# Performance work log

Hardware: AMD Instinct MI355X
Metric: run time of the kernel (lower is better)

Reference implementation:

```python
import jax, jax.numpy as jnp
import numpy as np

N_HEAD = 16


def _rope_tables(T, head_dim, dtype):
    # RotaryEmbedding buffers: freqs = outer(t, inv_freq), half-dim tables [T, head_dim//2]
    inv_freq = 1.0 / (10000.0 ** (jnp.arange(0, head_dim, 2, dtype=jnp.float32) / head_dim))
    freqs = jnp.arange(T, dtype=jnp.float32)[:, None] * inv_freq[None, :]
    return jnp.cos(freqs).astype(dtype), jnp.sin(freqs).astype(dtype)


def _apply_rotary(x, cos, sin):
    # x: [B,H,T,D]; cos/sin: [T,D//2] broadcast over B,H
    d = x.shape[-1] // 2
    x1, x2 = x[..., :d], x[..., d:]
    return jnp.concatenate([x1 * cos - x2 * sin, x2 * cos + x1 * sin], axis=-1)


def setup_inputs() -> dict:
    key = jax.random.key(0)
    k1, k2, k3 = jax.random.split(key, 3)
    B, T, C = 2, 2048, 2048
    x = jax.random.normal(k1, (B, T, C), dtype=jnp.float32)
    Wqkv = jax.random.normal(k2, (C, 3 * C), dtype=jnp.float32) * (1.0 / np.sqrt(C))
    Wproj = jax.random.normal(k3, (C, C), dtype=jnp.float32) * (1.0 / np.sqrt(C))
    return {"x": x, "Wqkv": Wqkv, "Wproj": Wproj}


def reference(x, Wqkv, Wproj):
    B, T, C = x.shape
    H = N_HEAD
    D = C // H
    qkv = (x @ Wqkv).reshape(B, T, 3, H, D)
    q, k, v = qkv[:, :, 0], qkv[:, :, 1], qkv[:, :, 2]  # [B,T,H,D]
    q = jnp.transpose(q, (0, 2, 1, 3))  # [B,H,T,D]
    k = jnp.transpose(k, (0, 2, 1, 3))
    v = jnp.transpose(v, (0, 2, 1, 3))
    cos, sin = _rope_tables(T, D, x.dtype)
    q = _apply_rotary(q, cos, sin)
    k = _apply_rotary(k, cos, sin)
    scale = 1.0 / np.sqrt(D)
    scores = jnp.einsum('bhqd,bhkd->bhqk', q, k) * scale
    causal = jnp.tril(jnp.ones((T, T), dtype=bool))
    scores = jnp.where(causal, scores, jnp.finfo(scores.dtype).min)
    attn = jax.nn.softmax(scores, axis=-1)
    out = jnp.einsum('bhqk,bhkd->bhqd', attn, v)
    out = jnp.transpose(out, (0, 2, 1, 3)).reshape(B, T, C)
    return out @ Wproj
```

## Files before the change

kernel.cpp:

```cpp
#include <hip/hip_runtime.h>
#include <hip/hip_bf16.h>

typedef short s16b;
using bf16x4 = __attribute__((ext_vector_type(4))) short;
using bf16x8 = __attribute__((ext_vector_type(8))) short;
using f32x4  = __attribute__((ext_vector_type(4))) float;
using u32x4  = __attribute__((ext_vector_type(4))) unsigned;

#define DEVINL __device__ __forceinline__

DEVINL float bf2f(short u) {
    union { float f; unsigned u; } x;
    x.u = ((unsigned)(unsigned short)u) << 16;
    return x.f;
}
DEVINL short f2bf(float f) {
    unsigned u = __builtin_bit_cast(unsigned, f);
    u += 0x7FFFu + ((u >> 16) & 1u);
    return (short)(u >> 16);
}
DEVINL unsigned cvtpk(float a, float b) {
    unsigned r;
    asm("v_cvt_pk_bf16_f32 %0, %1, %2" : "=v"(r) : "v"(a), "v"(b));
    return r;
}

DEVINL f32x4 mfma16(bf16x8 a, bf16x8 b, f32x4 c) {
    return __builtin_amdgcn_mfma_f32_16x16x32_bf16(a, b, c, 0, 0, 0);
}

DEVINL void gload_lds16(const void* g, void* lds_uniform) {
    __builtin_amdgcn_global_load_lds(
        (const __attribute__((address_space(1))) char*)(const char*)g,
        (__attribute__((address_space(3))) char*)(char*)lds_uniform, 16, 0, 0);
}

DEVINL int perm32(int k) {
    return ((k >> 2) & 3) * 8 + ((k >> 4) & 1) * 4 + (k & 3);
}

DEVINL bf16x8 lds128(const s16b* base, int row, int ks, int g) {
    const char* p = (const char*)base + row * 128 + ((((ks << 2) + g) ^ (row & 7)) << 4);
    return *(const bf16x8*)p;
}
DEVINL bf16x8 lds256(const s16b* base, int row, int ds, int g) {
    const char* p = (const char*)base + row * 256 + ((((ds << 2) + g) ^ (row & 7)) << 4);
    return *(const bf16x8*)p;
}

__global__ void k_tables(float* __restrict__ ctab, float* __restrict__ stab) {
    int idx = blockIdx.x * 256 + threadIdx.x;
    int i = idx & 63, t = idx >> 6;
    float inv = powf(10000.0f, -(float)i * (1.0f / 64.0f));
    float fr = (float)t * inv;
    ctab[idx] = cosf(fr);
    stab[idx] = sinf(fr);
}

__global__ void k_cvt_x(const float* __restrict__ x, s16b* __restrict__ xb) {
    int idx = blockIdx.x * 256 + threadIdx.x;
    int p = idx * 4;
    int row = p >> 11, pc = p & 2047;
    int grp = pc >> 5, sp = pc & 31;
    int c = sp >> 3, half = (sp >> 2) & 1;
    int ksrc = grp * 32 + half * 16 + c * 4;
    float4 v = *(const float4*)(x + (size_t)row * 2048 + ksrc);
    bf16x4 o;
    o[0] = f2bf(v.x); o[1] = f2bf(v.y); o[2] = f2bf(v.z); o[3] = f2bf(v.w);
    *(bf16x4*)(xb + (size_t)row * 2048 + pc) = o;
}

__global__ void k_tcvt(const float* __restrict__ in, s16b* __restrict__ out, int R, int C) {
    __shared__ float tile[32][33];
    int tx = threadIdx.x & 31, ty = threadIdx.x >> 5;
    int c0 = blockIdx.x * 32, r0 = blockIdx.y * 32;
#pragma unroll
    for (int kk = 0; kk < 4; ++kk) {
        int r = ty + kk * 8;
        tile[r][tx] = in[(size_t)(r0 + r) * C + c0 + tx];
    }
    __syncthreads();
#pragma unroll
    for (int kk = 0; kk < 4; ++kk) {
        int r = ty + kk * 8;
        out[(size_t)(c0 + r) * R + r0 + perm32(tx)] = f2bf(tile[tx][r]);
    }
}

#define STG_B01(DB, KB)                                                        \
  gload_lds16(srcB + (KB), lds + 49152 + (DB) * 32768 + tid16);                \
  gload_lds16(srcB + 262144 + (KB), lds + 49152 + (DB) * 32768 + 8192 + tid16);
#define STG_B23(DB, KB)                                                        \
  gload_lds16(srcB + 524288 + (KB), lds + 49152 + (DB) * 32768 + 16384 + tid16); \
  gload_lds16(srcB + 786432 + (KB), lds + 49152 + (DB) * 32768 + 24576 + tid16);
#define STG_A01(DB, KB)                                                        \
  gload_lds16(srcA + (KB), lds + (DB) * 16384 + tid16);                        \
  gload_lds16(srcA + 262144 + (KB), lds + (DB) * 16384 + 8192 + tid16);

#define AF_READ(B, KS)                                                         \
    _Pragma("unroll")                                                          \
    for (int fi = 0; fi < 4; ++fi) {                                           \
      int row = (fi >> 1) * 64 + wm * 32 + (fi & 1) * 16 + r15;                \
      af[fi] = *(const bf16x8*)(lds + (B) * 16384 + row * 128                  \
               + ((((KS) * 4 + g) ^ (row & 7)) << 4));                         \
    }

#define PH4(B, KH, JH, STGC, WN)                                               \
  {                                                                            \
    if ((JH) == 0) { AF_READ(B, KH) }                                          \
    _Pragma("unroll")                                                          \
    for (int fj = 0; fj < 2; ++fj) {                                           \
      int row = (JH) * 128 + wn * 32 + fj * 16 + r15;                          \
      bfr[fj] = *(const bf16x8*)(lds + 49152 + (B) * 32768 + row * 128         \
                + ((((KH) * 4 + g) ^ (row & 7)) << 4));                        \
    }                                                                          \
    STGC                                                                       \
    if ((WN) == 6) { asm volatile("s_waitcnt vmcnt(6)" ::: "memory");          \
                     __builtin_amdgcn_sched_barrier(0); }                      \
    else if ((WN) == 0) { asm volatile("s_waitcnt vmcnt(0)" ::: "memory");     \
                     __builtin_amdgcn_sched_barrier(0); }                      \
    __builtin_amdgcn_s_barrier();                                              \
    asm volatile("s_waitcnt lgkmcnt(0)" ::: "memory");                         \
    __builtin_amdgcn_sched_barrier(0);                                         \
    __builtin_amdgcn_s_setprio(1);                                             \
    _Pragma("unroll")                                                          \
    for (int fi = 0; fi < 4; ++fi)                                             \
      _Pragma("unroll")                                                        \
      for (int fj = 0; fj < 2; ++fj)                                           \
        acc[fi][(JH) * 2 + fj] = mfma16(af[fi], bfr[fj], acc[fi][(JH) * 2 + fj]); \
    __builtin_amdgcn_s_setprio(0);                                             \
    __builtin_amdgcn_s_barrier();                                              \
    __builtin_amdgcn_sched_barrier(0);                                         \
  }

#define DO_TILE3(B, S1, S2, S3, WNL)                                           \
    PH4(B, 0, 0, S1, -1)                                                       \
    PH4(B, 0, 1, S2, -1)                                                       \
    PH4(B, 1, 0, S3, -1)                                                       \
    PH4(B, 1, 1, , WNL)

#define GEMM3_MAINLOOP(A_, B_)                                                 \
    __shared__ __attribute__((aligned(16))) char lds[147456];                  \
    const int tid = threadIdx.x;                                               \
    const int lane = tid & 63, wave = tid >> 6;                                \
    const int g = lane >> 4, r15 = lane & 15;                                  \
    const int wm = wave >> 2, wn = wave & 3;                                   \
    const int tid16 = tid << 4;                                                \
    const int rowL = tid16 >> 7;                                               \
    const int swzL = ((((tid16 >> 4) & 7) ^ (rowL & 7)) << 4);                 \
    const char* srcA = (const char*)(A_) + (size_t)(bm + rowL) * 4096 + swzL;  \
    const char* srcB = (const char*)(B_) + (size_t)(bn + rowL) * 4096 + swzL;  \
    f32x4 acc[4][4] = {};                                                      \
    bf16x8 af[4], bfr[2];                                                      \
    STG_B01(0, 0) STG_A01(0, 0) STG_B23(0, 0)                                  \
    STG_B01(1, 128) STG_A01(1, 128) STG_B23(1, 128)                            \
    asm volatile("s_waitcnt vmcnt(6)" ::: "memory");                           \
    __builtin_amdgcn_sched_barrier(0);                                         \
    __builtin_amdgcn_s_barrier();                                              \
    for (int t3 = 0; t3 < 10; ++t3) {                                          \
        const int kb2 = (3 * t3 + 2) * 128;                                    \
        const int kb3 = kb2 + 128, kb4 = kb2 + 256;                            \
        DO_TILE3(0, STG_B01(2, kb2), STG_A01(2, kb2), STG_B23(2, kb2), 6)      \
        DO_TILE3(1, STG_B01(0, kb3), STG_A01(0, kb3), STG_B23(0, kb3), 6)      \
        DO_TILE3(2, STG_B01(1, kb4), STG_A01(1, kb4), STG_B23(1, kb4), 6)      \
    }                                                                          \
    DO_TILE3(0, , , , 0)                                                       \
    DO_TILE3(1, , , , -1)

__global__ __launch_bounds__(512) void k_gemm_qkv(
    const s16b* __restrict__ A, const s16b* __restrict__ Bt,
    s16b* __restrict__ Qb, s16b* __restrict__ Kp, s16b* __restrict__ Vt,
    const float* __restrict__ ctab, const float* __restrict__ stab) {
    const int bid = blockIdx.x;
    const int xcd = bid & 7, local = bid >> 3;
    const int rr_ = local >> 5, w = local & 31;
    const int bm = ((xcd & 3) * 8 + (w >> 2)) * 128;
    const int bn = ((xcd >> 2) * 12 + rr_ * 4 + (w & 3)) * 256;
    GEMM3_MAINLOOP(A, Bt)
    const int which = bn >> 11;
    if (which < 2) {
        char* sml = (char*)lds;
#pragma unroll
        for (int i = 0; i < 4; ++i) {
#pragma unroll
            for (int j = 0; j < 4; ++j) {
                int mb0 = (i >> 1) * 64 + wm * 32 + (i & 1) * 16 + 4 * g;
                int nn = (j >> 1) * 128 + wn * 32 + (j & 1) * 16 + r15;
#pragma unroll
                for (int e = 0; e < 4; ++e) {
                    int mm = mb0 + e;
                    *(s16b*)(sml + mm * 528 + ((nn * 2) ^ ((mm & 3) << 5))) =
                        f2bf(acc[i][j][e]);
                }
            }
        }
        __syncthreads();
        const int mrow = tid >> 2, c4 = tid & 3;
        const int bb = bm >> 11;
        const int tt = (bm & 2047) + mrow;
        const char* srow = sml + mrow * 528;
        const int sw = (mrow & 3) << 5;
        bf16x8 v[8];
#pragma unroll
        for (int k = 0; k < 8; ++k) {
            int lc = c4 + 4 * k;
            v[k] = *(const bf16x8*)(srow + ((lc * 16) ^ sw));
        }
        float cs[2][8], sn[2][8];
#pragma unroll
        for (int j = 0; j < 2; ++j) {
            int d0 = 8 * c4 + 32 * j;
            const float* cp = ctab + tt * 64 + d0;
            const float* sp = stab + tt * 64 + d0;
            *(float4*)&cs[j][0] = *(const float4*)cp;
            *(float4*)&cs[j][4] = *(const float4*)(cp + 4);
            *(float4*)&sn[j][0] = *(const float4*)sp;
            *(float4*)&sn[j][4] = *(const float4*)(sp + 4);
        }
        if (which == 0) {
            const float SC = 0.12751744154f;
#pragma unroll
            for (int j = 0; j < 2; ++j)
#pragma unroll
                for (int e = 0; e < 8; ++e) { cs[j][e] *= SC; sn[j][e] *= SC; }
        }
        bf16x8 o[8];
#pragma unroll
        for (int hh = 0; hh < 2; ++hh)
#pragma unroll
            for (int j = 0; j < 2; ++j) {
                int kl = hh * 4 + j, kh = kl + 2;
                bf16x8 r1, r2;
#pragma unroll
                for (int e = 0; e < 8; ++e) {
                    float c = cs[j][e], s = sn[j][e];
                    float x1 = bf2f(v[kl][e]), x2 = bf2f(v[kh][e]);
                    r1[e] = f2bf(x1 * c - x2 * s);
                    r2[e] = f2bf(x2 * c + x1 * s);
                }
                o[kl] = r1; o[kh] = r2;
            }
        if (which == 0) {
#pragma unroll
            for (int k = 0; k < 8; ++k) {
                int lc = c4 + 4 * k;
                int ng = bn + lc * 8;
                int h = (ng >> 7) & 15, d = ng & 127;
                *(bf16x8*)(Qb + ((size_t)(bb * 16 + h) * 2048 + tt) * 128 + d) = o[k];
            }
        } else {
#pragma unroll
            for (int k = 0; k < 8; ++k) {
                int lc = c4 + 4 * k;
                int ng = bn + lc * 8;
                int h = (ng >> 7) & 15, d = ng & 127;
                size_t base = ((size_t)(bb * 16 + h) * 2048 + tt) * 128 + (d & ~31);
                int w2 = d & 31;
                bf16x4 lo, hi;
#pragma unroll
                for (int e = 0; e < 4; ++e) { lo[e] = o[k][e]; hi[e] = o[k][e + 4]; }
                *(bf16x4*)(Kp + base + perm32(w2)) = lo;
                *(bf16x4*)(Kp + base + perm32(w2 + 4)) = hi;
            }
        }
    } else {
#pragma unroll
        for (int i = 0; i < 4; ++i) {
            int m0 = bm + (i >> 1) * 64 + wm * 32 + (i & 1) * 16 + 4 * g;
            int b = m0 >> 11, t0 = m0 & 2047;
            int pt = (t0 & ~31) + perm32(t0 & 31);
#pragma unroll
            for (int j = 0; j < 4; ++j) {
                int n = bn + (j >> 1) * 128 + wn * 32 + (j & 1) * 16 + r15;
                int h = (n >> 7) & 15, d = n & 127;
                size_t base = ((size_t)(b * 16 + h) * 128 + d) * 2048 + pt;
                bf16x4 pk;
#pragma unroll
                for (int e = 0; e < 4; ++e) pk[e] = f2bf(acc[i][j][e]);
                *(bf16x4*)(Vt + base) = pk;
            }
        }
    }
}

__global__ __launch_bounds__(512) void k_gemm_proj(
    const s16b* __restrict__ A, const s16b* __restrict__ Bt, float* __restrict__ Co) {
    const int bid = blockIdx.x;
    const int xcd = bid & 7, local = bid >> 3;
    const int bm = (xcd * 4 + (local & 3)) * 128;
    const int bn = (local >> 2) * 256;
    GEMM3_MAINLOOP(A, Bt)
#pragma unroll
    for (int i = 0; i < 4; ++i) {
        int m0 = bm + (i >> 1) * 64 + wm * 32 + (i & 1) * 16 + 4 * g;
#pragma unroll
        for (int j = 0; j < 4; ++j) {
            int n = bn + (j >> 1) * 128 + wn * 32 + (j & 1) * 16 + r15;
#pragma unroll
            for (int e = 0; e < 4; ++e) Co[(size_t)(m0 + e) * 2048 + n] = acc[i][j][e];
        }
    }
}

__global__ __launch_bounds__(256) void k_attn(
    const s16b* __restrict__ Qb, const s16b* __restrict__ Kp,
    const s16b* __restrict__ Vt, s16b* __restrict__ AO) {
    __shared__ alignas(16) s16b Ks[2][64 * 128];
    __shared__ alignas(16) s16b Vs[2][128 * 64];
    const int tid = threadIdx.x;
    const int lane = tid & 63, wave = tid >> 6;
    const int g = lane >> 4, r15 = lane & 15;
    const int bh = blockIdx.x, pp = blockIdx.y;
    const s16b* Qg = Qb + (size_t)bh * 2048 * 128;
    const char* Kg = (const char*)(Kp + (size_t)bh * 2048 * 128);
    const char* Vg = (const char*)(Vt + (size_t)bh * 128 * 2048);
    const int b = bh >> 4, h = bh & 15;

#define ASTG(BUF, KT)                                                          \
    {                                                                          \
      const int k0s = (KT) * 64;                                               \
      _Pragma("unroll")                                                        \
      for (int rr = 0; rr < 4; ++rr) {                                         \
        int uo = (rr * 256 + wave * 64) * 16;                                  \
        int o = uo + lane * 16;                                                \
        {                                                                      \
          int row = o >> 8, sl = (o >> 4) & 15;                                \
          int sg = (sl ^ (row & 7)) << 4;                                      \
          gload_lds16(Kg + (size_t)(k0s + row) * 256 + sg,                     \
                      (char*)Ks + (BUF) * 16384 + uo);                         \
        }                                                                      \
        {                                                                      \
          int row = o >> 7, sl = (o >> 4) & 7;                                 \
          int sg = (sl ^ (row & 7)) << 4;                                      \
          gload_lds16(Vg + (size_t)row * 4096 + (size_t)k0s * 2 + sg,          \
                      (char*)Vs + (BUF) * 16384 + uo);                         \
        }                                                                      \
      }                                                                        \
    }

    for (int pass = 0; pass < 2; ++pass) {
        const int qt = pass ? pp : (15 - pp);
        const int q0 = qt * 128 + wave * 32;
        const int ktiles = qt * 2 + 2;

        ASTG(0, 0)

        bf16x8 qf[2][4];
#pragma unroll
        for (int qs = 0; qs < 2; ++qs)
#pragma unroll
            for (int ds = 0; ds < 4; ++ds) {
                const s16b* p = Qg + (size_t)(q0 + qs * 16 + r15) * 128 + ds * 32 + 4 * g;
                bf16x4 lo = *(const bf16x4*)p;
                bf16x4 hi = *(const bf16x4*)(p + 16);
                qf[qs][ds] = __builtin_shufflevector(lo, hi, 0, 1, 2, 3, 4, 5, 6, 7);
            }

        f32x4 ot[8][2] = {};
        float m_s[2] = {-3e38f, -3e38f};
        float l_s[2] = {0.f, 0.f};

        for (int kt = 0; kt < ktiles; ++kt) {
            const int k0 = kt * 64;
            if (kt + 1 < ktiles) {
                ASTG((kt + 1) & 1, kt + 1)
                asm volatile("s_waitcnt vmcnt(8)" ::: "memory");
            } else {
                asm volatile("s_waitcnt vmcnt(0)" ::: "memory");
            }
            __builtin_amdgcn_sched_barrier(0);
            __builtin_amdgcn_s_barrier();
            asm volatile("" ::: "memory");
            __builtin_amdgcn_sched_barrier(0);

            if (k0 <= q0 + 31) {
                const s16b* Kb_ = (const s16b*)((const char*)Ks + (kt & 1) * 16384);
                const s16b* Vb_ = (const s16b*)((const char*)Vs + (kt & 1) * 16384);
                f32x4 st[4][2] = {};
                __builtin_amdgcn_s_setprio(1);
#pragma unroll
                for (int ds = 0; ds < 4; ++ds) {
#pragma unroll
                    for (int ks = 0; ks < 4; ++ks) {
                        bf16x8 kf = lds256(Kb_, ks * 16 + r15, ds, g);
#pragma unroll
                        for (int qs = 0; qs < 2; ++qs)
                            st[ks][qs] = mfma16(kf, qf[qs][ds], st[ks][qs]);
                    }
                }
                __builtin_amdgcn_s_setprio(0);
                if (k0 + 63 > q0) {
#pragma unroll
                    for (int ks = 0; ks < 4; ++ks)
#pragma unroll
                        for (int qs = 0; qs < 2; ++qs)
#pragma unroll
                            for (int e = 0; e < 4; ++e) {
                                int kk = k0 + ks * 16 + 4 * g + e;
                                int qq = q0 + qs * 16 + r15;
                                if (kk > qq) st[ks][qs][e] = -3e38f;
                            }
                }
#pragma unroll
                for (int qs = 0; qs < 2; ++qs) {
                    float mx = st[0][qs][0];
#pragma unroll
                    for (int ks = 0; ks < 4; ++ks)
#pragma unroll
                        for (int e = 0; e < 4; ++e)
                            if (ks | e) mx = fmaxf(mx, st[ks][qs][e]);
                    mx = fmaxf(mx, __shfl_xor(mx, 16));
                    mx = fmaxf(mx, __shfl_xor(mx, 32));
                    if (__any(mx > m_s[qs] + 8.f)) {
                        float mn = fmaxf(m_s[qs], mx);
                        float sf = exp2f(m_s[qs] - mn);
                        m_s[qs] = mn;
                        l_s[qs] *= sf;
#pragma unroll
                        for (int d8 = 0; d8 < 8; ++d8)
#pragma unroll
                            for (int e = 0; e < 4; ++e) ot[d8][qs][e] *= sf;
                    }
                    float mm = m_s[qs], sum = 0.f;
#pragma unroll
                    for (int ks = 0; ks < 4; ++ks)
#pragma unroll
                        for (int e = 0; e < 4; ++e) {
                            float p = exp2f(st[ks][qs][e] - mm);
                            st[ks][qs][e] = p;
                            sum += p;
                        }
                    l_s[qs] += sum;
                }
                bf16x8 pb[2][2];
#pragma unroll
                for (int k2 = 0; k2 < 2; ++k2)
#pragma unroll
                    for (int qs = 0; qs < 2; ++qs) {
                        u32x4 t;
                        t[0] = cvtpk(st[2 * k2][qs][0], st[2 * k2][qs][1]);
                        t[1] = cvtpk(st[2 * k2][qs][2], st[2 * k2][qs][3]);
                        t[2] = cvtpk(st[2 * k2 + 1][qs][0], st[2 * k2 + 1][qs][1]);
                        t[3] = cvtpk(st[2 * k2 + 1][qs][2], st[2 * k2 + 1][qs][3]);
                        pb[k2][qs] = __builtin_bit_cast(bf16x8, t);
                    }
                __builtin_amdgcn_s_setprio(1);
#pragma unroll
                for (int k2 = 0; k2 < 2; ++k2)
#pragma unroll
                    for (int d8 = 0; d8 < 8; ++d8) {
                        bf16x8 vf = lds128(Vb_, d8 * 16 + r15, k2, g);
#pragma unroll
                        for (int qs = 0; qs < 2; ++qs)
                            ot[d8][qs] = mfma16(vf, pb[k2][qs], ot[d8][qs]);
                    }
                __builtin_amdgcn_s_setprio(0);
            }
            asm volatile("" ::: "memory");
            __builtin_amdgcn_sched_barrier(0);
            __builtin_amdgcn_s_barrier();
        }
#pragma unroll
        for (int qs = 0; qs < 2; ++qs) {
            float l = l_s[qs];
            l += __shfl_xor(l, 16);
            l += __shfl_xor(l, 32);
            float inv = 1.0f / l;
            int q = q0 + qs * 16 + r15;
#pragma unroll
            for (int d8 = 0; d8 < 8; ++d8) {
                uint2 pk2;
                pk2.x = cvtpk(ot[d8][qs][0] * inv, ot[d8][qs][1] * inv);
                pk2.y = cvtpk(ot[d8][qs][2] * inv, ot[d8][qs][3] * inv);
                size_t off = ((size_t)(b * 2048 + q)) * 2048
                           + h * 128 + (d8 >> 1) * 32 + g * 8 + (d8 & 1) * 4;
                *(uint2*)(AO + off) = pk2;
            }
        }
    }
#undef ASTG
}

extern "C" void kernel_launch(void* const* d_in, const int* in_sizes, int n_in,
                              void* d_out, int out_size, void* d_ws, size_t ws_size,
                              hipStream_t stream) {
    const float* x = (const float*)d_in[0];
    const float* Wqkv = (const float*)d_in[1];
    const float* Wproj = (const float*)d_in[2];
    float* out = (float*)d_out;

    char* ws = (char*)d_ws;
    float* ctab = (float*)ws;
    float* stab = ctab + 2048 * 64;
    size_t off = 1048576;
    s16b* xb = (s16b*)(ws + off); off += 16777216;
    s16b* wqkvt = (s16b*)(ws + off); off += 25165824;
    s16b* wprojt = (s16b*)(ws + off); off += 8388608;
    s16b* Qb = (s16b*)(ws + off); off += 16777216;
    s16b* Kp = (s16b*)(ws + off); off += 16777216;
    s16b* Vt = (s16b*)(ws + off); off += 16777216;
    s16b* AO = xb;

    k_tables<<<dim3(512), dim3(256), 0, stream>>>(ctab, stab);
    k_cvt_x<<<dim3(8192), dim3(256), 0, stream>>>(x, xb);
    k_tcvt<<<dim3(192, 64), dim3(256), 0, stream>>>(Wqkv, wqkvt, 2048, 6144);
    k_tcvt<<<dim3(64, 64), dim3(256), 0, stream>>>(Wproj, wprojt, 2048, 2048);
    k_gemm_qkv<<<dim3(768), dim3(512), 0, stream>>>(xb, wqkvt, Qb, Kp, Vt, ctab, stab);
    k_attn<<<dim3(32, 8), dim3(256), 0, stream>>>(Qb, Kp, Vt, AO);
    k_gemm_proj<<<dim3(256), dim3(512), 0, stream>>>(AO, wprojt, out);
}
```

Measured before the change: 260.1 us.

## Merge preprocessing launches and split attention query tile across eight waves

```diff
diff --git a/kernel.cpp b/kernel.cpp
--- a/kernel.cpp
+++ b/kernel.cpp
@@ -48,32 +48,39 @@
     return *(const bf16x8*)p;
 }
 
-__global__ void k_tables(float* __restrict__ ctab, float* __restrict__ stab) {
-    int idx = blockIdx.x * 256 + threadIdx.x;
-    int i = idx & 63, t = idx >> 6;
-    float inv = powf(10000.0f, -(float)i * (1.0f / 64.0f));
-    float fr = (float)t * inv;
-    ctab[idx] = cosf(fr);
-    stab[idx] = sinf(fr);
-}
-
-__global__ void k_cvt_x(const float* __restrict__ x, s16b* __restrict__ xb) {
-    int idx = blockIdx.x * 256 + threadIdx.x;
-    int p = idx * 4;
-    int row = p >> 11, pc = p & 2047;
-    int grp = pc >> 5, sp = pc & 31;
-    int c = sp >> 3, half = (sp >> 2) & 1;
-    int ksrc = grp * 32 + half * 16 + c * 4;
-    float4 v = *(const float4*)(x + (size_t)row * 2048 + ksrc);
-    bf16x4 o;
-    o[0] = f2bf(v.x); o[1] = f2bf(v.y); o[2] = f2bf(v.z); o[3] = f2bf(v.w);
-    *(bf16x4*)(xb + (size_t)row * 2048 + pc) = o;
-}
-
-__global__ void k_tcvt(const float* __restrict__ in, s16b* __restrict__ out, int R, int C) {
+__global__ void k_pre(const float* __restrict__ x, s16b* __restrict__ xb,
+                      float* __restrict__ ctab, float* __restrict__ stab) {
+    int bid = blockIdx.x;
+    if (bid < 512) {
+        int idx = bid * 256 + threadIdx.x;
+        int i = idx & 63, t = idx >> 6;
+        float inv = powf(10000.0f, -(float)i * (1.0f / 64.0f));
+        float fr = (float)t * inv;
+        ctab[idx] = cosf(fr);
+        stab[idx] = sinf(fr);
+    } else {
+        int idx = (bid - 512) * 256 + threadIdx.x;
+        int p = idx * 4;
+        int row = p >> 11, pc = p & 2047;
+        int grp = pc >> 5, sp = pc & 31;
+        int c = sp >> 3, half = (sp >> 2) & 1;
+        int ksrc = grp * 32 + half * 16 + c * 4;
+        float4 v = *(const float4*)(x + (size_t)row * 2048 + ksrc);
+        bf16x4 o;
+        o[0] = f2bf(v.x); o[1] = f2bf(v.y); o[2] = f2bf(v.z); o[3] = f2bf(v.w);
+        *(bf16x4*)(xb + (size_t)row * 2048 + pc) = o;
+    }
+}
+
+__global__ void k_tcvt2(const float* __restrict__ Wqkv, s16b* __restrict__ wqkvt,
+                        const float* __restrict__ Wproj, s16b* __restrict__ wprojt) {
     __shared__ float tile[32][33];
+    int bx = blockIdx.x;
+    const float* in; s16b* out; int C, c0;
+    if (bx < 192) { in = Wqkv; out = wqkvt; C = 6144; c0 = bx * 32; }
+    else          { in = Wproj; out = wprojt; C = 2048; c0 = (bx - 192) * 32; }
     int tx = threadIdx.x & 31, ty = threadIdx.x >> 5;
-    int c0 = blockIdx.x * 32, r0 = blockIdx.y * 32;
+    int r0 = blockIdx.y * 32;
 #pragma unroll
     for (int kk = 0; kk < 4; ++kk) {
         int r = ty + kk * 8;
@@ -83,7 +90,7 @@
 #pragma unroll
     for (int kk = 0; kk < 4; ++kk) {
         int r = ty + kk * 8;
-        out[(size_t)(c0 + r) * R + r0 + perm32(tx)] = f2bf(tile[tx][r]);
+        out[(size_t)(c0 + r) * 2048 + r0 + perm32(tx)] = f2bf(tile[tx][r]);
     }
 }
 
@@ -302,7 +309,7 @@
     }
 }
 
-__global__ __launch_bounds__(256) void k_attn(
+__global__ __launch_bounds__(512) void k_attn(
     const s16b* __restrict__ Qb, const s16b* __restrict__ Kp,
     const s16b* __restrict__ Vt, s16b* __restrict__ AO) {
     __shared__ alignas(16) s16b Ks[2][64 * 128];
@@ -320,8 +327,8 @@
     {                                                                          \
       const int k0s = (KT) * 64;                                               \
       _Pragma("unroll")                                                        \
-      for (int rr = 0; rr < 4; ++rr) {                                         \
-        int uo = (rr * 256 + wave * 64) * 16;                                  \
+      for (int rr = 0; rr < 2; ++rr) {                                         \
+        int uo = (rr * 512 + wave * 64) * 16;                                  \
         int o = uo + lane * 16;                                                \
         {                                                                      \
           int row = o >> 8, sl = (o >> 4) & 15;                                \
@@ -340,31 +347,29 @@
 
     for (int pass = 0; pass < 2; ++pass) {
         const int qt = pass ? pp : (15 - pp);
-        const int q0 = qt * 128 + wave * 32;
+        const int q0 = qt * 128 + wave * 16;
         const int ktiles = qt * 2 + 2;
 
         ASTG(0, 0)
 
-        bf16x8 qf[2][4];
-#pragma unroll
-        for (int qs = 0; qs < 2; ++qs)
-#pragma unroll
-            for (int ds = 0; ds < 4; ++ds) {
-                const s16b* p = Qg + (size_t)(q0 + qs * 16 + r15) * 128 + ds * 32 + 4 * g;
-                bf16x4 lo = *(const bf16x4*)p;
-                bf16x4 hi = *(const bf16x4*)(p + 16);
-                qf[qs][ds] = __builtin_shufflevector(lo, hi, 0, 1, 2, 3, 4, 5, 6, 7);
-            }
-
-        f32x4 ot[8][2] = {};
-        float m_s[2] = {-3e38f, -3e38f};
-        float l_s[2] = {0.f, 0.f};
+        bf16x8 qf[4];
+#pragma unroll
+        for (int ds = 0; ds < 4; ++ds) {
+            const s16b* p = Qg + (size_t)(q0 + r15) * 128 + ds * 32 + 4 * g;
+            bf16x4 lo = *(const bf16x4*)p;
+            bf16x4 hi = *(const bf16x4*)(p + 16);
+            qf[ds] = __builtin_shufflevector(lo, hi, 0, 1, 2, 3, 4, 5, 6, 7);
+        }
+
+        f32x4 ot[8] = {};
+        float m_s = -3e38f;
+        float l_s = 0.f;
 
         for (int kt = 0; kt < ktiles; ++kt) {
             const int k0 = kt * 64;
             if (kt + 1 < ktiles) {
                 ASTG((kt + 1) & 1, kt + 1)
-                asm volatile("s_waitcnt vmcnt(8)" ::: "memory");
+                asm volatile("s_waitcnt vmcnt(4)" ::: "memory");
             } else {
                 asm volatile("s_waitcnt vmcnt(0)" ::: "memory");
             }
@@ -373,19 +378,17 @@
             asm volatile("" ::: "memory");
             __builtin_amdgcn_sched_barrier(0);
 
-            if (k0 <= q0 + 31) {
+            if (k0 <= q0 + 15) {
                 const s16b* Kb_ = (const s16b*)((const char*)Ks + (kt & 1) * 16384);
                 const s16b* Vb_ = (const s16b*)((const char*)Vs + (kt & 1) * 16384);
-                f32x4 st[4][2] = {};
+                f32x4 st[4] = {};
                 __builtin_amdgcn_s_setprio(1);
 #pragma unroll
                 for (int ds = 0; ds < 4; ++ds) {
 #pragma unroll
                     for (int ks = 0; ks < 4; ++ks) {
                         bf16x8 kf = lds256(Kb_, ks * 16 + r15, ds, g);
-#pragma unroll
-                        for (int qs = 0; qs < 2; ++qs)
-                            st[ks][qs] = mfma16(kf, qf[qs][ds], st[ks][qs]);
+                        st[ks] = mfma16(kf, qf[ds], st[ks]);
                     }
                 }
                 __builtin_amdgcn_s_setprio(0);
@@ -393,66 +396,59 @@
 #pragma unroll
                     for (int ks = 0; ks < 4; ++ks)
 #pragma unroll
-                        for (int qs = 0; qs < 2; ++qs)
-#pragma unroll
-                            for (int e = 0; e < 4; ++e) {
-                                int kk = k0 + ks * 16 + 4 * g + e;
-                                int qq = q0 + qs * 16 + r15;
-                                if (kk > qq) st[ks][qs][e] = -3e38f;
-                            }
+                        for (int e = 0; e < 4; ++e) {
+                            int kk = k0 + ks * 16 + 4 * g + e;
+                            int qq = q0 + r15;
+                            if (kk > qq) st[ks][e] = -3e38f;
+                        }
                 }
-#pragma unroll
-                for (int qs = 0; qs < 2; ++qs) {
-                    float mx = st[0][qs][0];
+                {
+                    float mx = st[0][0];
 #pragma unroll
                     for (int ks = 0; ks < 4; ++ks)
 #pragma unroll
                         for (int e = 0; e < 4; ++e)
-                            if (ks | e) mx = fmaxf(mx, st[ks][qs][e]);
+                            if (ks | e) mx = fmaxf(mx, st[ks][e]);
                     mx = fmaxf(mx, __shfl_xor(mx, 16));
                     mx = fmaxf(mx, __shfl_xor(mx, 32));
-                    if (__any(mx > m_s[qs] + 8.f)) {
-                        float mn = fmaxf(m_s[qs], mx);
-                        float sf = exp2f(m_s[qs] - mn);
-                        m_s[qs] = mn;
-                        l_s[qs] *= sf;
+                    if (__any(mx > m_s + 8.f)) {
+                        float mn = fmaxf(m_s, mx);
+                        float sf = exp2f(m_s - mn);
+                        m_s = mn;
+                        l_s *= sf;
 #pragma unroll
                         for (int d8 = 0; d8 < 8; ++d8)
 #pragma unroll
-                            for (int e = 0; e < 4; ++e) ot[d8][qs][e] *= sf;
+                            for (int e = 0; e < 4; ++e) ot[d8][e] *= sf;
                     }
-                    float mm = m_s[qs], sum = 0.f;
+                    float mm = m_s, sum = 0.f;
 #pragma unroll
                     for (int ks = 0; ks < 4; ++ks)
 #pragma unroll
                         for (int e = 0; e < 4; ++e) {
-                            float p = exp2f(st[ks][qs][e] - mm);
-                            st[ks][qs][e] = p;
+                            float p = exp2f(st[ks][e] - mm);
+                            st[ks][e] = p;
                             sum += p;
                         }
-                    l_s[qs] += sum;
+                    l_s += sum;
                 }
-                bf16x8 pb[2][2];
-#pragma unroll
-                for (int k2 = 0; k2 < 2; ++k2)
-#pragma unroll
-                    for (int qs = 0; qs < 2; ++qs) {
-                        u32x4 t;
-                        t[0] = cvtpk(st[2 * k2][qs][0], st[2 * k2][qs][1]);
-                        t[1] = cvtpk(st[2 * k2][qs][2], st[2 * k2][qs][3]);
-                        t[2] = cvtpk(st[2 * k2 + 1][qs][0], st[2 * k2 + 1][qs][1]);
-                        t[3] = cvtpk(st[2 * k2 + 1][qs][2], st[2 * k2 + 1][qs][3]);
-                        pb[k2][qs] = __builtin_bit_cast(bf16x8, t);
-                    }
+                bf16x8 pb[2];
+#pragma unroll
+                for (int k2 = 0; k2 < 2; ++k2) {
+                    u32x4 t;
+                    t[0] = cvtpk(st[2 * k2][0], st[2 * k2][1]);
+                    t[1] = cvtpk(st[2 * k2][2], st[2 * k2][3]);
+                    t[2] = cvtpk(st[2 * k2 + 1][0], st[2 * k2 + 1][1]);
+                    t[3] = cvtpk(st[2 * k2 + 1][2], st[2 * k2 + 1][3]);
+                    pb[k2] = __builtin_bit_cast(bf16x8, t);
+                }
                 __builtin_amdgcn_s_setprio(1);
 #pragma unroll
                 for (int k2 = 0; k2 < 2; ++k2)
 #pragma unroll
                     for (int d8 = 0; d8 < 8; ++d8) {
                         bf16x8 vf = lds128(Vb_, d8 * 16 + r15, k2, g);
-#pragma unroll
-                        for (int qs = 0; qs < 2; ++qs)
-                            ot[d8][qs] = mfma16(vf, pb[k2][qs], ot[d8][qs]);
+                        ot[d8] = mfma16(vf, pb[k2], ot[d8]);
                     }
                 __builtin_amdgcn_s_setprio(0);
             }
@@ -460,18 +456,17 @@
             __builtin_amdgcn_sched_barrier(0);
             __builtin_amdgcn_s_barrier();
         }
-#pragma unroll
-        for (int qs = 0; qs < 2; ++qs) {
-            float l = l_s[qs];
+        {
+            float l = l_s;
             l += __shfl_xor(l, 16);
             l += __shfl_xor(l, 32);
             float inv = 1.0f / l;
-            int q = q0 + qs * 16 + r15;
+            int q = q0 + r15;
 #pragma unroll
             for (int d8 = 0; d8 < 8; ++d8) {
                 uint2 pk2;
-                pk2.x = cvtpk(ot[d8][qs][0] * inv, ot[d8][qs][1] * inv);
-                pk2.y = cvtpk(ot[d8][qs][2] * inv, ot[d8][qs][3] * inv);
+                pk2.x = cvtpk(ot[d8][0] * inv, ot[d8][1] * inv);
+                pk2.y = cvtpk(ot[d8][2] * inv, ot[d8][3] * inv);
                 size_t off = ((size_t)(b * 2048 + q)) * 2048
                            + h * 128 + (d8 >> 1) * 32 + g * 8 + (d8 & 1) * 4;
                 *(uint2*)(AO + off) = pk2;
@@ -501,11 +496,9 @@
     s16b* Vt = (s16b*)(ws + off); off += 16777216;
     s16b* AO = xb;
 
-    k_tables<<<dim3(512), dim3(256), 0, stream>>>(ctab, stab);
-    k_cvt_x<<<dim3(8192), dim3(256), 0, stream>>>(x, xb);
-    k_tcvt<<<dim3(192, 64), dim3(256), 0, stream>>>(Wqkv, wqkvt, 2048, 6144);
-    k_tcvt<<<dim3(64, 64), dim3(256), 0, stream>>>(Wproj, wprojt, 2048, 2048);
+    k_pre<<<dim3(8704), dim3(256), 0, stream>>>(x, xb, ctab, stab);
+    k_tcvt2<<<dim3(256, 64), dim3(256), 0, stream>>>(Wqkv, wqkvt, Wproj, wprojt);
     k_gemm_qkv<<<dim3(768), dim3(512), 0, stream>>>(xb, wqkvt, Qb, Kp, Vt, ctab, stab);
-    k_attn<<<dim3(32, 8), dim3(256), 0, stream>>>(Qb, Kp, Vt, AO);
+    k_attn<<<dim3(32, 8), dim3(512), 0, stream>>>(Qb, Kp, Vt, AO);
     k_gemm_proj<<<dim3(256), dim3(512), 0, stream>>>(AO, wprojt, out);
 }
```

Measured after the change: 239.2 us. -8.0%, faster.
